# Kernel tuning notes

Measured on AMD Instinct MI355X. Metric: run time of the kernel, lower is better.

Reference implementation:

```python
import jax, jax.numpy as jnp
import numpy as np
from jax import lax

ALPHA = 0.1
N = 1024      # gallery size
J = 4         # number of embed blocks (2048 / 512)
BLOCK = 512

def setup_inputs() -> dict:
    key = jax.random.key(0)
    k1, k2, k3, k4 = jax.random.split(key, 4)
    x = jax.random.normal(k1, (N, 1024), dtype=jnp.float32)
    Wb = jax.random.normal(k2, (1024, 2048), dtype=jnp.float32) / np.sqrt(1024.0)
    W_embed = jax.random.normal(k3, (J, BLOCK, BLOCK, 2), dtype=jnp.float32) / BLOCK
    b_embed = jax.random.normal(k4, (J, 2), dtype=jnp.float32)
    return {"x": x, "Wb": Wb, "W_embed": W_embed, "b_embed": b_embed}

def _forward(x, Wb, W_embed, b_embed):
    alpha = ALPHA
    feats = x @ Wb                                   # [N, 2048]
    n = feats.shape[0]
    xb = feats.reshape(n, J, BLOCK).transpose(1, 0, 2)  # [J, N, BLOCK]
    # pairwise bilinear scores per block: S[j, a, b, k] = x_j[a] W_jk x_j[b] + b_jk
    S = jnp.einsum('jac,jcdk,jbd->jabk', xb, W_embed, xb) + b_embed[:, None, None, :]
    # transition matrices built from detached scores (g_g_score.data.clone())
    Sg = lax.stop_gradient(S)
    diag_mask = jnp.eye(n, dtype=bool)[None, :, :, None]     # [1, N, N, 1]
    masked = jnp.where(diag_mask, -jnp.inf, Sg)
    A = jax.nn.softmax(masked, axis=2)               # row softmax, [J, N, N, 2]
    A = jnp.transpose(A, (0, 3, 1, 2))               # [J, 2, N, N]
    I_N = jnp.eye(n, dtype=S.dtype)
    # closed-form personalized-PageRank diffusion, batched over (J, 2)
    A_an = (1.0 - alpha) * jnp.linalg.inv(I_N - alpha * A)  # [J, 2, N, N]
    # s[a,c] = sum_b p[a,b] * A[c,b]  (torch: p @ A.T)
    one = alpha * jnp.einsum('jabk,ikcb->jiack', S, A) + (1.0 - alpha) * S[:, None]
    ana = jnp.einsum('jabk,ikcb->jiack', S, A_an)
    out = jnp.concatenate([one.reshape(J, J, n * n, 2),
                           ana.reshape(J, J, n * n, 2)], axis=2)
    return out.reshape(-1, 2)

def reference(x, Wb, W_embed, b_embed):
    return _forward(x, Wb, W_embed, b_embed)
```

## Files before the change

### kernel.cpp

```cpp
#include <hip/hip_runtime.h>

#define NDIM 1024
#define NN (1024ull*1024ull)
#define MB (1ull<<20)

using f32x4  = __attribute__((ext_vector_type(4))) float;
using bf16x8 = __attribute__((ext_vector_type(8))) __bf16;
using u16x8  = __attribute__((ext_vector_type(8))) unsigned short;

__device__ __forceinline__ float bf2f(unsigned short u){
  union{unsigned int i; float f;} x; x.i = ((unsigned int)u)<<16; return x.f;
}
__device__ __forceinline__ unsigned short f2bf(float f){
  union{float fl; unsigned int i;} u; u.fl = f;
  unsigned int x = u.i;
  return (unsigned short)((x + 0x7fffu + ((x>>16)&1u)) >> 16);
}

__device__ __forceinline__ void gload16(const unsigned short* g, unsigned short* l){
  __builtin_amdgcn_global_load_lds(
      (const __attribute__((address_space(1))) void*)g,
      (__attribute__((address_space(3))) void*)l,
      16, 0, 0);
}


__global__ void k_split_x(const float* __restrict__ x, unsigned short* __restrict__ hi,
                          unsigned short* __restrict__ lo){
  size_t idx = ((size_t)blockIdx.x*256 + threadIdx.x)*4;
  float4 v = *(const float4*)(x+idx);
  float vv[4] = {v.x, v.y, v.z, v.w};
  ushort4 h, l;
  unsigned short* hp = (unsigned short*)&h;
  unsigned short* lp = (unsigned short*)&l;
  #pragma unroll
  for (int s=0;s<4;s++){
    unsigned short hb = f2bf(vv[s]);
    hp[s] = hb;
    lp[s] = f2bf(vv[s] - bf2f(hb));
  }
  *(ushort4*)(hi+idx) = h;
  *(ushort4*)(lo+idx) = l;
}

__global__ void k_trans_split(const float* __restrict__ Wb, unsigned short* __restrict__ hi,
                              unsigned short* __restrict__ lo){
  __shared__ float t[32][33];
  int bd = blockIdx.x, bc = blockIdx.y;
  int tx = threadIdx.x, ty = threadIdx.y;
  #pragma unroll
  for (int r=0;r<4;r++){
    int c = bc*32 + ty + r*8;
    t[ty+r*8][tx] = Wb[(size_t)c*2048 + bd*32 + tx];
  }
  __syncthreads();
  #pragma unroll
  for (int r=0;r<4;r++){
    int d = bd*32 + ty + r*8, c = bc*32 + tx;
    float v = t[tx][ty+r*8];
    unsigned short h = f2bf(v);
    hi[(size_t)d*1024 + c] = h;
    lo[(size_t)d*1024 + c] = f2bf(v - bf2f(h));
  }
}

__global__ void k_wt(const float* __restrict__ W, unsigned short* __restrict__ WT){
  __shared__ float t[32][33];
  int z = blockIdx.z; int j = z>>1, k = z&1;
  int bd = blockIdx.x, bc = blockIdx.y;
  int tx = threadIdx.x, ty = threadIdx.y;
  #pragma unroll
  for (int r=0;r<4;r++){
    int c = bc*32 + ty + r*8, d = bd*32 + tx;
    t[ty+r*8][tx] = W[(((size_t)j*512 + c)*512 + d)*2 + k];
  }
  __syncthreads();
  #pragma unroll
  for (int r=0;r<4;r++){
    int d = bd*32 + ty + r*8, c = bc*32 + tx;
    WT[((size_t)z*512 + d)*512 + c] = f2bf(t[tx][ty+r*8]);
  }
}

__global__ void k_softmax(const unsigned short* __restrict__ S, unsigned short* __restrict__ A){
  int z = blockIdx.y, c = blockIdx.x, t = threadIdx.x;
  const unsigned short* row = S + ((size_t)z*NDIM + c)*NDIM;
  __shared__ float red[256];
  float v[4];
  float mx = -1e30f;
  #pragma unroll
  for (int s=0;s<4;s++){
    int b = t + s*256;
    float x = bf2f(row[b]);
    if (b==c) x = -1e30f;
    v[s] = x; mx = fmaxf(mx, x);
  }
  red[t]=mx; __syncthreads();
  for (int o=128;o>0;o>>=1){ if (t<o) red[t]=fmaxf(red[t],red[t+o]); __syncthreads(); }
  mx = red[0]; __syncthreads();
  float e[4]; float sum=0.f;
  #pragma unroll
  for (int s=0;s<4;s++){ e[s] = __expf(v[s]-mx); sum += e[s]; }
  red[t]=sum; __syncthreads();
  for (int o=128;o>0;o>>=1){ if (t<o) red[t]+=red[t+o]; __syncthreads(); }
  sum = red[0];
  float inv = 1.0f/sum;
  unsigned short* Ar = A + ((size_t)z*NDIM + c)*NDIM;
  #pragma unroll
  for (int s=0;s<4;s++){
    int b = t + s*256;
    Ar[b] = f2bf(e[s]*inv);
  }
}

__global__ void k_transb(const unsigned short* __restrict__ A, unsigned short* __restrict__ AT){
  __shared__ unsigned short t[64][65];
  int z = blockIdx.z, bb = blockIdx.x, bc = blockIdx.y;
  int tx = threadIdx.x, ty = threadIdx.y;
  const unsigned short* Az = A + (size_t)z*NN;
  #pragma unroll
  for (int r=0;r<16;r++){
    int c = bc*64 + ty + r*4;
    t[ty+r*4][tx] = Az[(size_t)c*NDIM + bb*64 + tx];
  }
  __syncthreads();
  unsigned short* Tz = AT + (size_t)z*NN;
  #pragma unroll
  for (int r=0;r<16;r++){
    int b = bb*64 + ty + r*4;
    Tz[(size_t)b*NDIM + bc*64 + tx] = t[tx][ty+r*4];
  }
}

__global__ void k_combine(const unsigned short* __restrict__ A, const unsigned short* __restrict__ A2,
                          const unsigned short* __restrict__ A3, unsigned short* __restrict__ Aan){
  size_t idx = ((size_t)blockIdx.x*256 + threadIdx.x)*8;
  int cb = (int)(idx & (NN - 1));
  int c = cb >> 10, b0 = cb & 1023;
  u16x8 a  = *(const u16x8*)(A+idx);
  u16x8 a2 = *(const u16x8*)(A2+idx);
  u16x8 a3 = *(const u16x8*)(A3+idx);
  u16x8 o;
  #pragma unroll
  for (int s=0;s<8;s++){
    float v = 0.1f*bf2f(a[s]) + 0.01f*bf2f(a2[s]) + 0.001f*bf2f(a3[s]);
    if (b0+s == c) v += 1.0f;
    o[s] = f2bf(0.9f*v);
  }
  *(u16x8*)(Aan+idx) = o;
}


struct GemmP {
  const unsigned short* Aseg[3]; const unsigned short* Bseg[3];
  long long sA, sB;
  int zShiftA, zShiftB;
  int lda, ldb;
  int K, tilesN;
  unsigned short* Cb; long long sCb; int ldcb;
  const float* bias;
  float scale;
};

template<int NSEG>
__global__ __launch_bounds__(256) void k_gemm(GemmP p){
  const int z = blockIdx.y;
  const int tm = blockIdx.x / p.tilesN;
  const int tn = blockIdx.x % p.tilesN;
  const size_t zoffA = (size_t)(z>>p.zShiftA)*(size_t)p.sA;
  const size_t zoffB = (size_t)(z>>p.zShiftB)*(size_t)p.sB;
  __shared__ unsigned short As[2][4096];
  __shared__ unsigned short Bs[2][4096];
  const int t = threadIdx.x;
  const int lane = t & 63;
  const int w = t >> 6;
  const int wm = w >> 1, wn = w & 1;

  f32x4 acc[4][4];
  #pragma unroll
  for (int m=0;m<4;m++)
    #pragma unroll
    for (int n=0;n<4;n++)
      acc[m][n] = (f32x4)(0.0f);

  const int srow = w*32 + (lane>>2);
  const int swz  = ((lane&3) ^ ((srow>>1)&3)) * 8;
  const size_t aoff0 = (size_t)(tm*128 + srow)*p.lda + swz;
  const size_t aoff1 = (size_t)(tm*128 + srow + 16)*p.lda + swz;
  const size_t boff0 = (size_t)(tn*128 + srow)*p.ldb + swz;
  const size_t boff1 = (size_t)(tn*128 + srow + 16)*p.ldb + swz;

  const int kpseg = p.K >> 5;
  const int nt = kpseg * NSEG;

  auto stage = [&](int step, int buf){
    const int seg = (NSEG==1) ? 0 : (step / kpseg);
    const int k0 = (step - seg*kpseg) << 5;
    const unsigned short* ga = p.Aseg[seg] + zoffA;
    const unsigned short* gb = p.Bseg[seg] + zoffB;
    gload16(ga + aoff0 + k0, &As[buf][w*1024]);
    gload16(ga + aoff1 + k0, &As[buf][w*1024+512]);
    gload16(gb + boff0 + k0, &Bs[buf][w*1024]);
    gload16(gb + boff1 + k0, &Bs[buf][w*1024+512]);
  };

  const int rb = lane & 15, g = lane >> 4;
  const int rswz = (g ^ ((rb>>1)&3)) * 8;

  stage(0, 0);
  __syncthreads();
  int cur = 0;
  for (int s=0; s<nt; ++s){
    if (s+1 < nt) stage(s+1, cur^1);
    bf16x8 af[4], bfr[4];
    #pragma unroll
    for (int m=0;m<4;m++) af[m]  = *(const bf16x8*)&As[cur][(wm*64 + m*16 + rb)*32 + rswz];
    #pragma unroll
    for (int n=0;n<4;n++) bfr[n] = *(const bf16x8*)&Bs[cur][(wn*64 + n*16 + rb)*32 + rswz];
    #pragma unroll
    for (int m=0;m<4;m++)
      #pragma unroll
      for (int n=0;n<4;n++)
        acc[m][n] = __builtin_amdgcn_mfma_f32_16x16x32_bf16(af[m], bfr[n], acc[m][n], 0, 0, 0);
    __syncthreads();
    cur ^= 1;
  }

  const int rl = (lane>>4)*4;
  const int cl = lane & 15;
  const int row0 = tm*128 + wm*64;
  const int col0 = tn*128 + wn*64;
  const float bz = p.bias ? p.bias[z] : 0.0f;
  #pragma unroll
  for (int m=0;m<4;m++)
    #pragma unroll
    for (int n=0;n<4;n++)
      #pragma unroll
      for (int r=0;r<4;r++){
        const int row = row0 + m*16 + rl + r;
        const int col = col0 + n*16 + cl;
        p.Cb[(size_t)z*p.sCb + (size_t)row*p.ldcb + col] = f2bf(p.scale*acc[m][n][r] + bz);
      }
}

struct OutP {
  const unsigned short* Sp;
  const unsigned short* Bp;
  float* outp;
};

template<bool WITH_S>
__global__ __launch_bounds__(256,2) void k_out(OutP p){
  const int zi = blockIdx.y;
  const int jj = zi >> 2, ii = zi & 3;
  const int tm = blockIdx.x >> 3, tn = blockIdx.x & 7;
  const unsigned short* A0 = p.Sp + (size_t)(jj*2+0)*NN;
  const unsigned short* A1 = p.Sp + (size_t)(jj*2+1)*NN;
  const unsigned short* B0 = p.Bp + (size_t)(ii*2+0)*NN;
  const unsigned short* B1 = p.Bp + (size_t)(ii*2+1)*NN;
  __shared__ unsigned short As[2][2][4096];
  __shared__ unsigned short Bs[2][2][4096];
  const int t = threadIdx.x;
  const int lane = t & 63;
  const int w = t >> 6;
  const int wm = w >> 1, wn = w & 1;

  f32x4 acc0[4][4], acc1[4][4];
  #pragma unroll
  for (int m=0;m<4;m++)
    #pragma unroll
    for (int n=0;n<4;n++){
      acc0[m][n] = (f32x4)(0.0f);
      acc1[m][n] = (f32x4)(0.0f);
    }

  const int srow = w*32 + (lane>>2);
  const int swz  = ((lane&3) ^ ((srow>>1)&3)) * 8;
  const size_t aoff0 = (size_t)(tm*128 + srow)*1024 + swz;
  const size_t aoff1 = (size_t)(tm*128 + srow + 16)*1024 + swz;
  const size_t boff0 = (size_t)(tn*128 + srow)*1024 + swz;
  const size_t boff1 = (size_t)(tn*128 + srow + 16)*1024 + swz;

  auto stage = [&](int step, int buf){
    const int k0 = step << 5;
    gload16(A0 + aoff0 + k0, &As[buf][0][w*1024]);
    gload16(A0 + aoff1 + k0, &As[buf][0][w*1024+512]);
    gload16(A1 + aoff0 + k0, &As[buf][1][w*1024]);
    gload16(A1 + aoff1 + k0, &As[buf][1][w*1024+512]);
    gload16(B0 + boff0 + k0, &Bs[buf][0][w*1024]);
    gload16(B0 + boff1 + k0, &Bs[buf][0][w*1024+512]);
    gload16(B1 + boff0 + k0, &Bs[buf][1][w*1024]);
    gload16(B1 + boff1 + k0, &Bs[buf][1][w*1024+512]);
  };

  const int rb = lane & 15, g = lane >> 4;
  const int rswz = (g ^ ((rb>>1)&3)) * 8;

  stage(0, 0);
  __syncthreads();
  int cur = 0;
  for (int s=0; s<32; ++s){
    if (s+1 < 32) stage(s+1, cur^1);
    {
      bf16x8 af[4], bfr[4];
      #pragma unroll
      for (int m=0;m<4;m++) af[m]  = *(const bf16x8*)&As[cur][0][(wm*64 + m*16 + rb)*32 + rswz];
      #pragma unroll
      for (int n=0;n<4;n++) bfr[n] = *(const bf16x8*)&Bs[cur][0][(wn*64 + n*16 + rb)*32 + rswz];
      #pragma unroll
      for (int m=0;m<4;m++)
        #pragma unroll
        for (int n=0;n<4;n++)
          acc0[m][n] = __builtin_amdgcn_mfma_f32_16x16x32_bf16(af[m], bfr[n], acc0[m][n], 0, 0, 0);
    }
    {
      bf16x8 af[4], bfr[4];
      #pragma unroll
      for (int m=0;m<4;m++) af[m]  = *(const bf16x8*)&As[cur][1][(wm*64 + m*16 + rb)*32 + rswz];
      #pragma unroll
      for (int n=0;n<4;n++) bfr[n] = *(const bf16x8*)&Bs[cur][1][(wn*64 + n*16 + rb)*32 + rswz];
      #pragma unroll
      for (int m=0;m<4;m++)
        #pragma unroll
        for (int n=0;n<4;n++)
          acc1[m][n] = __builtin_amdgcn_mfma_f32_16x16x32_bf16(af[m], bfr[n], acc1[m][n], 0, 0, 0);
    }
    __syncthreads();
    cur ^= 1;
  }

  const int rl = (lane>>4)*4;
  const int cl = lane & 15;
  const int row0 = tm*128 + wm*64;
  const int col0 = tn*128 + wn*64;
  const size_t ob = (size_t)(jj*4+ii)*(4ull*NN) + (WITH_S ? 0 : 2ull*NN);
  #pragma unroll
  for (int m=0;m<4;m++)
    #pragma unroll
    for (int n=0;n<4;n++)
      #pragma unroll
      for (int r=0;r<4;r++){
        const int row = row0 + m*16 + rl + r;
        const int col = col0 + n*16 + cl;
        float v0 = acc0[m][n][r];
        float v1 = acc1[m][n][r];
        if (WITH_S){
          v0 = 0.1f*v0 + 0.9f*bf2f(A0[(size_t)row*1024 + col]);
          v1 = 0.1f*v1 + 0.9f*bf2f(A1[(size_t)row*1024 + col]);
        }
        float2 val; val.x = v0; val.y = v1;
        *(float2*)(p.outp + ob + ((size_t)row*1024 + col)*2) = val;
      }
}


extern "C" void kernel_launch(void* const* d_in, const int* in_sizes, int n_in,
                              void* d_out, int out_size, void* d_ws, size_t ws_size,
                              hipStream_t stream){
  (void)in_sizes; (void)n_in; (void)out_size; (void)ws_size;
  const float* x  = (const float*)d_in[0];
  const float* Wb = (const float*)d_in[1];
  const float* We = (const float*)d_in[2];
  const float* be = (const float*)d_in[3];
  float* out = (float*)d_out;
  char* ws = (char*)d_ws;

  unsigned short* xhi   = (unsigned short*)(ws + 0);
  unsigned short* xlo   = (unsigned short*)(ws + 2*MB);
  unsigned short* wbth  = (unsigned short*)(ws + 4*MB);
  unsigned short* wbtl  = (unsigned short*)(ws + 8*MB);
  unsigned short* featb = (unsigned short*)(ws + 12*MB);
  unsigned short* WT    = (unsigned short*)(ws + 16*MB);
  unsigned short* Tb    = (unsigned short*)(ws + 20*MB);
  unsigned short* Sb    = (unsigned short*)(ws + 28*MB);
  unsigned short* Abuf  = (unsigned short*)(ws + 44*MB);
  unsigned short* ATb   = (unsigned short*)(ws + 60*MB);
  unsigned short* A2b   = (unsigned short*)(ws + 76*MB);
  unsigned short* A3b   = (unsigned short*)(ws + 92*MB);
  unsigned short* Aan   = (unsigned short*)(ws + 108*MB);

  k_split_x<<<dim3(1024), dim3(256), 0, stream>>>(x, xhi, xlo);
  k_trans_split<<<dim3(64,32), dim3(32,8), 0, stream>>>(Wb, wbth, wbtl);
  k_wt<<<dim3(16,16,8), dim3(32,8), 0, stream>>>(We, WT);

  {
    GemmP q{};
    q.Aseg[0]=xhi; q.Bseg[0]=wbth;
    q.Aseg[1]=xhi; q.Bseg[1]=wbtl;
    q.Aseg[2]=xlo; q.Bseg[2]=wbth;
    q.sA = 0; q.sB = 0; q.zShiftA = 0; q.zShiftB = 0;
    q.lda = 1024; q.ldb = 1024; q.K = 1024; q.tilesN = 16;
    q.Cb = featb; q.sCb = 0; q.ldcb = 2048;
    q.bias = nullptr; q.scale = 1.0f;
    k_gemm<3><<<dim3(8*16,1), dim3(256), 0, stream>>>(q);
  }

  {
    GemmP q{};
    q.Aseg[0] = featb; q.sA = 512; q.zShiftA = 1; q.lda = 2048;
    q.Bseg[0] = WT;    q.sB = (long long)512*512; q.zShiftB = 0; q.ldb = 512;
    q.K = 512; q.tilesN = 4;
    q.Cb = Tb; q.sCb = (long long)1024*512; q.ldcb = 512;
    q.bias = nullptr; q.scale = 1.0f;
    k_gemm<1><<<dim3(8*4,8), dim3(256), 0, stream>>>(q);
  }

  {
    GemmP q{};
    q.Aseg[0] = Tb;    q.sA = (long long)1024*512; q.zShiftA = 0; q.lda = 512;
    q.Bseg[0] = featb; q.sB = 512; q.zShiftB = 1; q.ldb = 2048;
    q.K = 512; q.tilesN = 8;
    q.Cb = Sb; q.sCb = (long long)NN; q.ldcb = 1024;
    q.bias = be; q.scale = 1.0f;
    k_gemm<1><<<dim3(8*8,8), dim3(256), 0, stream>>>(q);
  }

  k_softmax<<<dim3(1024,8), dim3(256), 0, stream>>>(Sb, Abuf);
  k_transb<<<dim3(16,16,8), dim3(64,4), 0, stream>>>(Abuf, ATb);

  auto pgemm = [&](const unsigned short* Aop, unsigned short* dst){
    GemmP q{};
    q.Aseg[0] = Aop; q.sA = (long long)NN; q.zShiftA = 0; q.lda = 1024;
    q.Bseg[0] = ATb; q.sB = (long long)NN; q.zShiftB = 0; q.ldb = 1024;
    q.K = 1024; q.tilesN = 8;
    q.Cb = dst; q.sCb = (long long)NN; q.ldcb = 1024;
    q.bias = nullptr; q.scale = 1.0f;
    k_gemm<1><<<dim3(8*8,8), dim3(256), 0, stream>>>(q);
  };
  pgemm(Abuf, A2b);
  pgemm(A2b,  A3b);

  k_combine<<<dim3(4096), dim3(256), 0, stream>>>(Abuf, A2b, A3b, Aan);

  {
    OutP q{Sb, Abuf, out};
    k_out<true><<<dim3(64,16), dim3(256), 0, stream>>>(q);
  }
  {
    OutP q{Sb, Aan, out};
    k_out<false><<<dim3(64,16), dim3(256), 0, stream>>>(q);
  }
}
```

Before: 659.3 us.

## Enlarge k_out tiles to 256x128 with 512 threads and finer-grained pipeline sync

The output GEMM kernel moves from 256-thread blocks with 128x128 tiles to 512-thread blocks with 256x128 tiles, so each B tile loaded into LDS is reused across twice as many rows. Shared memory becomes one flat buffer, the two score channels are interleaved in the MFMA loop, and __syncthreads is replaced by explicit vmcnt waits, raw barriers and setprio around the MFMA block. The aim is to cut global/LDS traffic per FLOP and overlap the next stage's loads with compute. The cost is higher LDS use per block and fewer blocks in the grid.

```diff
diff --git a/kernel.cpp b/kernel.cpp
--- a/kernel.cpp
+++ b/kernel.cpp
@@ -243,6 +243,7 @@
       }
 }
 
+
 struct OutP {
   const unsigned short* Sp;
   const unsigned short* Bp;
@@ -250,20 +251,20 @@
 };
 
 template<bool WITH_S>
-__global__ __launch_bounds__(256,2) void k_out(OutP p){
+__global__ __launch_bounds__(512,2) void k_out(OutP p){
   const int zi = blockIdx.y;
   const int jj = zi >> 2, ii = zi & 3;
-  const int tm = blockIdx.x >> 3, tn = blockIdx.x & 7;
+  const int tm = blockIdx.x & 3;
+  const int tn = blockIdx.x >> 2;
   const unsigned short* A0 = p.Sp + (size_t)(jj*2+0)*NN;
   const unsigned short* A1 = p.Sp + (size_t)(jj*2+1)*NN;
   const unsigned short* B0 = p.Bp + (size_t)(ii*2+0)*NN;
   const unsigned short* B1 = p.Bp + (size_t)(ii*2+1)*NN;
-  __shared__ unsigned short As[2][2][4096];
-  __shared__ unsigned short Bs[2][2][4096];
+  __shared__ unsigned short sm[49152];
   const int t = threadIdx.x;
   const int lane = t & 63;
   const int w = t >> 6;
-  const int wm = w >> 1, wn = w & 1;
+  const int wr = w >> 1, wc = w & 1;
 
   f32x4 acc0[4][4], acc1[4][4];
   #pragma unroll
@@ -274,65 +275,74 @@
       acc1[m][n] = (f32x4)(0.0f);
     }
 
-  const int srow = w*32 + (lane>>2);
-  const int swz  = ((lane&3) ^ ((srow>>1)&3)) * 8;
-  const size_t aoff0 = (size_t)(tm*128 + srow)*1024 + swz;
-  const size_t aoff1 = (size_t)(tm*128 + srow + 16)*1024 + swz;
-  const size_t boff0 = (size_t)(tn*128 + srow)*1024 + swz;
-  const size_t boff1 = (size_t)(tn*128 + srow + 16)*1024 + swz;
+  const int lrow = w*16 + (lane>>2);
+  const int rowA0 = lrow, rowA1 = 128 + lrow, rowB = lrow;
+  const int chA0 = ((lane&3) ^ ((rowA0>>1)&3)) * 8;
+  const int chA1 = ((lane&3) ^ ((rowA1>>1)&3)) * 8;
+  const int chB  = ((lane&3) ^ ((rowB>>1)&3)) * 8;
+  const size_t aoffc0 = (size_t)(tm*256 + rowA0)*1024 + chA0;
+  const size_t aoffc1 = (size_t)(tm*256 + rowA1)*1024 + chA1;
+  const size_t boff   = (size_t)(tn*128 + rowB)*1024 + chB;
+  const int wslot = w*512;
 
   auto stage = [&](int step, int buf){
     const int k0 = step << 5;
-    gload16(A0 + aoff0 + k0, &As[buf][0][w*1024]);
-    gload16(A0 + aoff1 + k0, &As[buf][0][w*1024+512]);
-    gload16(A1 + aoff0 + k0, &As[buf][1][w*1024]);
-    gload16(A1 + aoff1 + k0, &As[buf][1][w*1024+512]);
-    gload16(B0 + boff0 + k0, &Bs[buf][0][w*1024]);
-    gload16(B0 + boff1 + k0, &Bs[buf][0][w*1024+512]);
-    gload16(B1 + boff0 + k0, &Bs[buf][1][w*1024]);
-    gload16(B1 + boff1 + k0, &Bs[buf][1][w*1024+512]);
+    unsigned short* r0 = &sm[(buf*2+0)*12288];
+    unsigned short* r1 = &sm[(buf*2+1)*12288];
+    gload16(A0 + aoffc0 + k0, r0 + wslot);
+    gload16(A0 + aoffc1 + k0, r0 + 4096 + wslot);
+    gload16(B0 + boff   + k0, r0 + 8192 + wslot);
+    gload16(A1 + aoffc0 + k0, r1 + wslot);
+    gload16(A1 + aoffc1 + k0, r1 + 4096 + wslot);
+    gload16(B1 + boff   + k0, r1 + 8192 + wslot);
   };
 
   const int rb = lane & 15, g = lane >> 4;
   const int rswz = (g ^ ((rb>>1)&3)) * 8;
 
   stage(0, 0);
-  __syncthreads();
   int cur = 0;
   for (int s=0; s<32; ++s){
-    if (s+1 < 32) stage(s+1, cur^1);
-    {
-      bf16x8 af[4], bfr[4];
+    if (s+1 < 32){
+      stage(s+1, cur^1);
+      asm volatile("s_waitcnt vmcnt(6)" ::: "memory");
+    } else {
+      asm volatile("s_waitcnt vmcnt(0)" ::: "memory");
+    }
+    __builtin_amdgcn_s_barrier();
+    __builtin_amdgcn_sched_barrier(0);
+    const unsigned short* r0 = &sm[(cur*2+0)*12288];
+    const unsigned short* r1 = &sm[(cur*2+1)*12288];
+    bf16x8 af0[4], bf0[4], af1[4], bf1[4];
+    #pragma unroll
+    for (int m=0;m<4;m++){
+      af0[m] = *(const bf16x8*)(r0 + (wr*64 + m*16 + rb)*32 + rswz);
+      af1[m] = *(const bf16x8*)(r1 + (wr*64 + m*16 + rb)*32 + rswz);
+    }
+    #pragma unroll
+    for (int n=0;n<4;n++){
+      bf0[n] = *(const bf16x8*)(r0 + 8192 + (wc*64 + n*16 + rb)*32 + rswz);
+      bf1[n] = *(const bf16x8*)(r1 + 8192 + (wc*64 + n*16 + rb)*32 + rswz);
+    }
+    __builtin_amdgcn_s_setprio(1);
+    #pragma unroll
+    for (int m=0;m<4;m++)
       #pragma unroll
-      for (int m=0;m<4;m++) af[m]  = *(const bf16x8*)&As[cur][0][(wm*64 + m*16 + rb)*32 + rswz];
-      #pragma unroll
-      for (int n=0;n<4;n++) bfr[n] = *(const bf16x8*)&Bs[cur][0][(wn*64 + n*16 + rb)*32 + rswz];
-      #pragma unroll
-      for (int m=0;m<4;m++)
-        #pragma unroll
-        for (int n=0;n<4;n++)
-          acc0[m][n] = __builtin_amdgcn_mfma_f32_16x16x32_bf16(af[m], bfr[n], acc0[m][n], 0, 0, 0);
-    }
-    {
-      bf16x8 af[4], bfr[4];
-      #pragma unroll
-      for (int m=0;m<4;m++) af[m]  = *(const bf16x8*)&As[cur][1][(wm*64 + m*16 + rb)*32 + rswz];
-      #pragma unroll
-      for (int n=0;n<4;n++) bfr[n] = *(const bf16x8*)&Bs[cur][1][(wn*64 + n*16 + rb)*32 + rswz];
-      #pragma unroll
-      for (int m=0;m<4;m++)
-        #pragma unroll
-        for (int n=0;n<4;n++)
-          acc1[m][n] = __builtin_amdgcn_mfma_f32_16x16x32_bf16(af[m], bfr[n], acc1[m][n], 0, 0, 0);
-    }
-    __syncthreads();
+      for (int n=0;n<4;n++){
+        acc0[m][n] = __builtin_amdgcn_mfma_f32_16x16x32_bf16(af0[m], bf0[n], acc0[m][n], 0, 0, 0);
+        acc1[m][n] = __builtin_amdgcn_mfma_f32_16x16x32_bf16(af1[m], bf1[n], acc1[m][n], 0, 0, 0);
+      }
+    __builtin_amdgcn_s_setprio(0);
+    __builtin_amdgcn_sched_barrier(0);
+    __builtin_amdgcn_s_barrier();
+    __builtin_amdgcn_sched_barrier(0);
     cur ^= 1;
   }
 
   const int rl = (lane>>4)*4;
   const int cl = lane & 15;
-  const int row0 = tm*128 + wm*64;
-  const int col0 = tn*128 + wn*64;
+  const int row0 = tm*256 + wr*64;
+  const int col0 = tn*128 + wc*64;
   const size_t ob = (size_t)(jj*4+ii)*(4ull*NN) + (WITH_S ? 0 : 2ull*NN);
   #pragma unroll
   for (int m=0;m<4;m++)
@@ -434,10 +444,10 @@
 
   {
     OutP q{Sb, Abuf, out};
-    k_out<true><<<dim3(64,16), dim3(256), 0, stream>>>(q);
+    k_out<true><<<dim3(32,16), dim3(512), 0, stream>>>(q);
   }
   {
     OutP q{Sb, Aan, out};
-    k_out<false><<<dim3(64,16), dim3(256), 0, stream>>>(q);
-  }
-}
+    k_out<false><<<dim3(32,16), dim3(512), 0, stream>>>(q);
+  }
+}
```

Measured after the change: 610.8 us. 1.08x faster.
